# Kernel optimization log

Measured on AMD Instinct MI355X. Metric: run time of the kernel, lower is better.

## Reference

```python
import jax, jax.numpy as jnp
import numpy as np

N_EDGES = 4_000_000
EMBED_DIM = 64
N_CLAUSES = 1_000_000


def setup_inputs() -> dict:
    key = jax.random.key(0)
    k1, k2, k3, k4 = jax.random.split(key, 4)
    embeds = jax.random.normal(k1, (N_EDGES, EMBED_DIM), dtype=jnp.float32)
    weight = jax.random.normal(k2, (EMBED_DIM, 1), dtype=jnp.float32)
    # edge_feature is the literal sign in {-1, +1}
    edge_feature = (2 * jax.random.randint(k3, (N_EDGES, 1), 0, 2) - 1).astype(jnp.float32)
    # clause id of each edge (replaces the dense 0/1 function_mask rows)
    edge_clause = jax.random.randint(k4, (N_EDGES,), 0, N_CLAUSES, dtype=jnp.int32)
    return {
        "embeds": embeds,
        "weight": weight,
        "edge_feature": edge_feature,
        "edge_clause": edge_clause,
        "n_clauses": N_CLAUSES,
    }


def reference(embeds, weight, edge_feature, edge_clause, n_clauses):
    # scores = embeds.mm(self.weight)  -> [n_edges, 1]
    scores = embeds @ weight
    # edge_values = scores + (1 - edge_feature) / 2
    edge_values = scores + (1.0 - edge_feature) * 0.5
    # edge_values = (edge_values > 0.5).float()  (is_train=True branch)
    edge_values = (edge_values > 0.5).astype(jnp.float32)
    # clause_values = function_mask @ edge_values : 0/1 mask matmul == segment sum over clauses
    clause_values = jax.ops.segment_sum(edge_values, edge_clause, num_segments=n_clauses)
    # clause_values = (clause_values > 0).float()
    return (clause_values > 0).astype(jnp.float32)
```

## Files before the change

### kernel.cpp

```cpp
#include <hip/hip_runtime.h>


__global__ __launch_bounds__(256) void zero_out(float4* __restrict__ out4, int n4) {
    int i = blockIdx.x * blockDim.x + threadIdx.x;
    if (i < n4) out4[i] = make_float4(0.f, 0.f, 0.f, 0.f);
}

__global__ __launch_bounds__(256) void graphsage_edge_scatter(
    const float4* __restrict__ embeds4,
    const float*  __restrict__ weight,
    const float*  __restrict__ edge_feature,
    const int*    __restrict__ edge_clause,
    float*        __restrict__ out,
    int n_edges)
{
    const int lane = threadIdx.x & 63;
    const int sub  = lane & 15;
    const int grp  = lane >> 4;

    const int wave_id = (blockIdx.x * blockDim.x + threadIdx.x) >> 6;
    const int n_waves = (gridDim.x * blockDim.x) >> 6;

    const float4 w4 = ((const float4*)weight)[sub];

    for (int base = wave_id * 16; base < n_edges; base += n_waves * 16) {
        if (base + 16 <= n_edges) {
            float ef = 0.f; int cl = 0;
            if (lane < 16) {
                ef = edge_feature[base + lane];
                cl = edge_clause[base + lane];
            }

            const float4* p = embeds4 + base * 16 + lane;
            float4 v0 = p[0];
            float4 v1 = p[64];
            float4 v2 = p[128];
            float4 v3 = p[192];

            float s0 = v0.x*w4.x + v0.y*w4.y + v0.z*w4.z + v0.w*w4.w;
            float s1 = v1.x*w4.x + v1.y*w4.y + v1.z*w4.z + v1.w*w4.w;
            float s2 = v2.x*w4.x + v2.y*w4.y + v2.z*w4.z + v2.w*w4.w;
            float s3 = v3.x*w4.x + v3.y*w4.y + v3.z*w4.z + v3.w*w4.w;

#define RED16(s) do { s += __shfl_xor(s, 1); s += __shfl_xor(s, 2); \
                      s += __shfl_xor(s, 4); s += __shfl_xor(s, 8); } while (0)
            RED16(s0); RED16(s1); RED16(s2); RED16(s3);
#undef RED16

            int srcl = (lane & 3) << 4;
            float a0 = __shfl(s0, srcl);
            float a1 = __shfl(s1, srcl);
            float a2 = __shfl(s2, srcl);
            float a3 = __shfl(s3, srcl);
            int k = (lane >> 2) & 3;
            float sc = (k == 0) ? a0 : (k == 1) ? a1 : (k == 2) ? a2 : a3;

            if (lane < 16) {
                if (sc > 0.5f * ef) out[cl] = 1.0f;
            }
        } else {
            if (lane < 16) {
                int e = base + lane;
                if (e < n_edges) {
                    const float* row = (const float*)(embeds4 + e * 16);
                    float s = 0.f;
                    for (int j = 0; j < 64; ++j) s += row[j] * weight[j];
                    if (s > 0.5f * edge_feature[e]) out[edge_clause[e]] = 1.0f;
                }
            }
        }
    }
}

extern "C" void kernel_launch(void* const* d_in, const int* in_sizes, int n_in,
                              void* d_out, int out_size, void* d_ws, size_t ws_size,
                              hipStream_t stream) {
    const float* embeds       = (const float*)d_in[0];
    const float* weight       = (const float*)d_in[1];
    const float* edge_feature = (const float*)d_in[2];
    const int*   edge_clause  = (const int*)d_in[3];

    float* out = (float*)d_out;
    const int n_edges = in_sizes[3];

    const int n4 = out_size / 4;
    zero_out<<<(n4 + 255) / 256, 256, 0, stream>>>((float4*)out, n4);
    if (out_size % 4) {
    }

    const int block = 256;
    const int grid  = 4096;
    graphsage_edge_scatter<<<grid, block, 0, stream>>>(
        (const float4*)embeds, weight, edge_feature, edge_clause, out, n_edges);
}
```

Measured before the change: 1.291 ms.

## Switch to one-row-per-thread dot product with wave-uniform weights

New measurement: 1.306 ms. Within noise of the previous version (+1.1%).

```diff
diff --git a/kernel.cpp b/kernel.cpp
--- a/kernel.cpp
+++ b/kernel.cpp
@@ -6,7 +6,14 @@
     if (i < n4) out4[i] = make_float4(0.f, 0.f, 0.f, 0.f);
 }
 
-__global__ __launch_bounds__(256) void graphsage_edge_scatter(
+__device__ __forceinline__ float uniform_f(float x) {
+    union { float f; int i; } u;
+    u.f = x;
+    u.i = __builtin_amdgcn_readfirstlane(u.i);
+    return u.f;
+}
+
+__global__ __launch_bounds__(256) void graphsage_row_per_thread(
     const float4* __restrict__ embeds4,
     const float*  __restrict__ weight,
     const float*  __restrict__ edge_feature,
@@ -14,61 +21,40 @@
     float*        __restrict__ out,
     int n_edges)
 {
-    const int lane = threadIdx.x & 63;
-    const int sub  = lane & 15;
-    const int grp  = lane >> 4;
+    float w[64];
+#pragma unroll
+    for (int j = 0; j < 16; ++j) {
+        float4 t = ((const float4*)weight)[j];
+        w[4*j+0] = uniform_f(t.x);
+        w[4*j+1] = uniform_f(t.y);
+        w[4*j+2] = uniform_f(t.z);
+        w[4*j+3] = uniform_f(t.w);
+    }
 
-    const int wave_id = (blockIdx.x * blockDim.x + threadIdx.x) >> 6;
-    const int n_waves = (gridDim.x * blockDim.x) >> 6;
+    const int tid      = blockIdx.x * blockDim.x + threadIdx.x;
+    const int nthreads = gridDim.x * blockDim.x;
 
-    const float4 w4 = ((const float4*)weight)[sub];
+    for (int e = tid; e < n_edges; e += nthreads) {
+        const float4* __restrict__ row = embeds4 + (size_t)e * 16;
 
-    for (int base = wave_id * 16; base < n_edges; base += n_waves * 16) {
-        if (base + 16 <= n_edges) {
-            float ef = 0.f; int cl = 0;
-            if (lane < 16) {
-                ef = edge_feature[base + lane];
-                cl = edge_clause[base + lane];
-            }
+        float4 v[16];
+#pragma unroll
+        for (int j = 0; j < 16; ++j) v[j] = row[j];
 
-            const float4* p = embeds4 + base * 16 + lane;
-            float4 v0 = p[0];
-            float4 v1 = p[64];
-            float4 v2 = p[128];
-            float4 v3 = p[192];
+        const float ef = edge_feature[e];
+        const int   cl = edge_clause[e];
 
-            float s0 = v0.x*w4.x + v0.y*w4.y + v0.z*w4.z + v0.w*w4.w;
-            float s1 = v1.x*w4.x + v1.y*w4.y + v1.z*w4.z + v1.w*w4.w;
-            float s2 = v2.x*w4.x + v2.y*w4.y + v2.z*w4.z + v2.w*w4.w;
-            float s3 = v3.x*w4.x + v3.y*w4.y + v3.z*w4.z + v3.w*w4.w;
+        float s0 = 0.f, s1 = 0.f, s2 = 0.f, s3 = 0.f;
+#pragma unroll
+        for (int j = 0; j < 16; j += 4) {
+            s0 += v[j+0].x*w[4*j+0]  + v[j+0].y*w[4*j+1]  + v[j+0].z*w[4*j+2]  + v[j+0].w*w[4*j+3];
+            s1 += v[j+1].x*w[4*j+4]  + v[j+1].y*w[4*j+5]  + v[j+1].z*w[4*j+6]  + v[j+1].w*w[4*j+7];
+            s2 += v[j+2].x*w[4*j+8]  + v[j+2].y*w[4*j+9]  + v[j+2].z*w[4*j+10] + v[j+2].w*w[4*j+11];
+            s3 += v[j+3].x*w[4*j+12] + v[j+3].y*w[4*j+13] + v[j+3].z*w[4*j+14] + v[j+3].w*w[4*j+15];
+        }
+        const float s = (s0 + s1) + (s2 + s3);
 
-#define RED16(s) do { s += __shfl_xor(s, 1); s += __shfl_xor(s, 2); \
-                      s += __shfl_xor(s, 4); s += __shfl_xor(s, 8); } while (0)
-            RED16(s0); RED16(s1); RED16(s2); RED16(s3);
-#undef RED16
-
-            int srcl = (lane & 3) << 4;
-            float a0 = __shfl(s0, srcl);
-            float a1 = __shfl(s1, srcl);
-            float a2 = __shfl(s2, srcl);
-            float a3 = __shfl(s3, srcl);
-            int k = (lane >> 2) & 3;
-            float sc = (k == 0) ? a0 : (k == 1) ? a1 : (k == 2) ? a2 : a3;
-
-            if (lane < 16) {
-                if (sc > 0.5f * ef) out[cl] = 1.0f;
-            }
-        } else {
-            if (lane < 16) {
-                int e = base + lane;
-                if (e < n_edges) {
-                    const float* row = (const float*)(embeds4 + e * 16);
-                    float s = 0.f;
-                    for (int j = 0; j < 64; ++j) s += row[j] * weight[j];
-                    if (s > 0.5f * edge_feature[e]) out[edge_clause[e]] = 1.0f;
-                }
-            }
-        }
+        if (s > 0.5f * ef) out[cl] = 1.0f;
     }
 }
 
@@ -85,11 +71,9 @@
 
     const int n4 = out_size / 4;
     zero_out<<<(n4 + 255) / 256, 256, 0, stream>>>((float4*)out, n4);
-    if (out_size % 4) {
-    }
 
     const int block = 256;
-    const int grid  = 4096;
-    graphsage_edge_scatter<<<grid, block, 0, stream>>>(
+    const int grid  = 2048;
+    graphsage_row_per_thread<<<grid, block, 0, stream>>>(
         (const float4*)embeds, weight, edge_feature, edge_clause, out, n_edges);
 }
```
